# Performance work log

Measured on AMD Instinct MI355X. Metric: run time of the kernel, lower is better.

Reference implementation:

```python
import jax, jax.numpy as jnp
import numpy as np

B, C, L = 64, 128, 1024
SCALES = [8, 4, 2, 1]
EPS_BN = 1e-5


def _ema_vec(x_ds, alpha):
    # x_ds: [B, C, Ls]; alpha: [1, C, 1] in (0,1)
    Ls = x_ds.shape[-1]
    powers = jnp.arange(Ls - 1, -1, -1, dtype=x_ds.dtype)
    base = jnp.power(1.0 - alpha, powers)                                 # [1, C, Ls]
    w_num = jnp.concatenate([base[..., :1], base[..., 1:] * alpha], axis=-1)
    num = jnp.cumsum(x_ds * w_num, axis=-1)
    den = jnp.maximum(jnp.cumsum(base, axis=-1), 1e-12)
    return num / den


def _dwconv(x, w, s):
    # depthwise Conv1d: kernel 2s, stride s, pad s//2, groups=C, no bias
    return jax.lax.conv_general_dilated(
        x, w, window_strides=(s,), padding=[(s // 2, s // 2)],
        dimension_numbers=("NCH", "OIH", "NCH"), feature_group_count=C)


def _proj(v, w1, b1, w2, b2):
    # v: [B, C, Ls] -> Linear(Ls->L), exact GELU, Linear(L->L); torch Linear y = x @ W.T + b
    h = jax.nn.gelu(jnp.einsum("bcs,ls->bcl", v, w1) + b1, approximate=False)
    return jnp.einsum("bcl,ml->bcm", h, w2) + b2


def _hasd(x, bn_g, bn_b, branch, gate):
    Bn = x.shape[0]
    # BatchNorm1d over flattened (C*L) features, training-mode batch stats (biased var)
    v = x.reshape(Bn, C * L)
    mu = v.mean(axis=0)
    var = jnp.mean((v - mu) ** 2, axis=0)
    xn = (((v - mu) / jnp.sqrt(var + EPS_BN)) * bn_g + bn_b).reshape(Bn, C, L)
    trends, seasons, gates = [], [], []
    for s in SCALES:
        if s > 1:
            cw, w1, b1, w2, b2 = branch[s]
            down = _dwconv(xn, cw, s)                                     # [B, C, L//s]
            up = _proj(down, w1, b1, w2, b2)                              # [B, C, L]
        else:
            down = xn
            up = xn
        gw, gb, al = gate[s]
        alpha = jax.nn.sigmoid(al)
        trend_ds = _ema_vec(down, alpha)
        trend_up = _proj(trend_ds, w1, b1, w2, b2) if s > 1 else trend_ds
        season = up - trend_up
        trends.append(trend_up)
        seasons.append(season)
        gates.append(jax.nn.sigmoid(season.mean(axis=-1) @ gw.T + gb))    # [B, 1]
    g = jnp.concatenate(gates, axis=1)                                    # [B, n_scales]
    g = g / (g.sum(axis=1, keepdims=True) + 1e-6)
    g = g[:, :, None, None]
    trend_out = (jnp.stack(trends, axis=1) * g).sum(axis=1)
    season_out = (jnp.stack(seasons, axis=1) * g).sum(axis=1)
    return season_out, trend_out


def setup_inputs() -> dict:
    key = jax.random.key(0)
    ks = iter(jax.random.split(key, 64))
    d = {"x": jax.random.normal(next(ks), (B, C, L), jnp.float32)}
    d["bn_g"] = 1.0 + 0.1 * jax.random.normal(next(ks), (C * L,), jnp.float32)
    d["bn_b"] = 0.1 * jax.random.normal(next(ks), (C * L,), jnp.float32)
    for s in (8, 4, 2):
        Ls = L // s
        d[f"cw{s}"] = jax.random.normal(next(ks), (C, 1, 2 * s), jnp.float32) / np.sqrt(2 * s)
        d[f"w1_{s}"] = jax.random.normal(next(ks), (L, Ls), jnp.float32) / np.sqrt(Ls)
        d[f"b1_{s}"] = jnp.zeros((L,), jnp.float32)
        d[f"w2_{s}"] = jax.random.normal(next(ks), (L, L), jnp.float32) / np.sqrt(L)
        d[f"b2_{s}"] = jnp.zeros((L,), jnp.float32)
    for s in SCALES:
        d[f"gw{s}"] = jax.random.normal(next(ks), (1, C), jnp.float32) / np.sqrt(C)
        d[f"gb{s}"] = jnp.zeros((1,), jnp.float32)
        d[f"al{s}"] = jnp.full((1, C, 1), 0.3, jnp.float32)
    return d


def reference(x, bn_g, bn_b,
              cw8, w1_8, b1_8, w2_8, b2_8,
              cw4, w1_4, b1_4, w2_4, b2_4,
              cw2, w1_2, b1_2, w2_2, b2_2,
              gw8, gb8, al8, gw4, gb4, al4, gw2, gb2, al2, gw1, gb1, al1):
    branch = {8: (cw8, w1_8, b1_8, w2_8, b2_8),
              4: (cw4, w1_4, b1_4, w2_4, b2_4),
              2: (cw2, w1_2, b1_2, w2_2, b2_2)}
    gate = {8: (gw8, gb8, al8), 4: (gw4, gb4, al4),
            2: (gw2, gb2, al2), 1: (gw1, gb1, al1)}
    return _hasd(x, bn_g, bn_b, branch, gate)
```

## Files before the change

kernel.cpp:

```cpp
#include <hip/hip_runtime.h>
#include <hip/hip_bf16.h>
#include <math.h>

#define Bdim 64
#define Cdim 128
#define Ldim 1024
#define BC   (Bdim * Cdim)
#define CLn  (Cdim * Ldim)
#define TOT  (Bdim * CLn)

typedef unsigned short ushort_t;
typedef short s16x8 __attribute__((ext_vector_type(8)));
typedef float f32x4 __attribute__((ext_vector_type(4)));

__device__ __forceinline__ float bf2f(ushort_t u) {
    return __uint_as_float(((unsigned)u) << 16);
}
__device__ __forceinline__ ushort_t f2bf(float f) {
    __hip_bfloat16 h = __float2bfloat16(f);
    return *(ushort_t*)&h;
}
__device__ __forceinline__ void async16(const ushort_t* g, ushort_t* l) {
    __builtin_amdgcn_global_load_lds(
        (const __attribute__((address_space(1))) unsigned int*)g,
        (__attribute__((address_space(3))) unsigned int*)l, 16, 0, 0);
}
__device__ __forceinline__ float fast_gelu(float z) {
    float z2 = z * z;
    float inner = fmaf(0.044715f * z2, z, z);
    float e = __expf(-1.5957691216057308f * inner);
    return z * __builtin_amdgcn_rcpf(1.f + e);
}

#define PREP_CONV   15872
#define PREP_BN     (PREP_CONV + 512)
#define PREP_W2CS   (PREP_BN + 48)
#define PREP_COEF   (PREP_W2CS + 128)
#define PREP_TOTAL  (PREP_COEF + 128)

__global__ __launch_bounds__(256) void prep_kernel(
    const float* __restrict__ w1_8, const float* __restrict__ w1_4,
    const float* __restrict__ w1_2, const float* __restrict__ w2_8,
    const float* __restrict__ w2_4, const float* __restrict__ w2_2,
    ushort_t* __restrict__ wdst,
    const float* __restrict__ x, const float* __restrict__ bn_g,
    const float* __restrict__ bn_b, float* __restrict__ scale,
    float* __restrict__ shift,
    float* __restrict__ w2cs,
    const float* __restrict__ al1, const float* __restrict__ al2,
    const float* __restrict__ al4, const float* __restrict__ al8,
    float* __restrict__ coef, float* __restrict__ am,
    float* __restrict__ rs)
{
    __shared__ float red[4][64];
    int bid = blockIdx.x;
    int tid = threadIdx.x;

    if (bid < PREP_CONV) {
        int idx = bid * 256 + tid;
        const float* src; int off;
        if      (idx < 131072)  { src = w1_8; off = 0; }
        else if (idx < 393216)  { src = w1_4; off = 131072; }
        else if (idx < 917504)  { src = w1_2; off = 393216; }
        else if (idx < 1966080) { src = w2_8; off = 917504; }
        else if (idx < 3014656) { src = w2_4; off = 1966080; }
        else                    { src = w2_2; off = 3014656; }
        wdst[idx] = f2bf(src[idx - off]);
    } else if (bid < PREP_BN) {
        int f = (bid - PREP_CONV) * 256 + tid;
        float sum = 0.f, sumsq = 0.f;
        for (int b = 0; b < Bdim; ++b) {
            float v = x[(size_t)b * CLn + f];
            sum += v; sumsq += v * v;
        }
        float mu  = sum * (1.f / Bdim);
        float var = fmaxf(sumsq * (1.f / Bdim) - mu * mu, 0.f);
        float sc  = bn_g[f] / sqrtf(var + 1e-5f);
        scale[f] = sc;
        shift[f] = bn_b[f] - mu * sc;
    } else if (bid < PREP_W2CS) {
        int fl = bid - PREP_BN;
        int bx = fl & 15;
        int by = fl >> 4;
        const float* w = (by == 0) ? w2_8 : (by == 1) ? w2_4 : w2_2;
        int h  = bx * 64 + (tid & 63);
        int ls = tid >> 6;
        float s = 0.f;
        for (int l = ls; l < 1024; l += 4) s += w[(size_t)l * 1024 + h];
        red[ls][tid & 63] = s;
        __syncthreads();
        if (ls == 0)
            w2cs[by * 1024 + h] =
                red[0][tid] + red[1][tid] + red[2][tid] + red[3][tid];
    } else if (bid < PREP_COEF) {
        int c = bid - PREP_W2CS;
        const float* als[4] = {al1, al2, al4, al8};
        const int Lss[4]    = {1024, 512, 256, 128};
        const int offs[4]   = {0, 1024, 1536, 1792};
#pragma unroll
        for (int si = 0; si < 4; ++si) {
            double a  = 1.0 / (1.0 + exp(-(double)als[si][c]));
            double m  = 1.0 - a;
            double lm = log(m);
            int Ls = Lss[si];
            for (int t = tid; t < Ls; t += 256) {
                double dt  = (1.0 - exp((double)(t + 1) * lm)) / a;
                double den = exp((double)(Ls - 1 - t) * lm) * dt;
                double ramp = (den >= 1e-12) ? 1.0 : den * 1e12;
                coef[(size_t)c * 1920 + offs[si] + t] = (float)(ramp / dt);
            }
            if (tid == 0) {
                am[c * 8 + si * 2 + 0] = (float)a;
                am[c * 8 + si * 2 + 1] = (float)m;
            }
        }
    } else {
        int idx = (bid - PREP_COEF) * 256 + tid;
        rs[idx] = 0.f;
    }
}

template<int SEG>
__device__ __forceinline__ void ema_pass1(
    const float* __restrict__ src, float a, float m, bool lead,
    float* __restrict__ xs, float& Sp, float& Sm)
{
    int lane = threadIdx.x & 63;
    if constexpr (SEG >= 4) {
#pragma unroll
        for (int i = 0; i < SEG; i += 4) {
            f32x4 u = *(const f32x4*)&src[lane * SEG + i];
            xs[i + 0] = u.x; xs[i + 1] = u.y;
            xs[i + 2] = u.z; xs[i + 3] = u.w;
        }
    } else {
        float2 u = *(const float2*)&src[lane * 2];
        xs[0] = u.x; xs[1] = u.y;
    }
    float p = 0.f;
#pragma unroll
    for (int i = 0; i < SEG; ++i) {
        float bi = a * xs[i];
        if (lead && lane == 0 && i == 0) bi = xs[0];
        p = fmaf(m, p, bi);
    }
    float sm = m;
#pragma unroll
    for (int i = 1; i < SEG; ++i) sm *= m;
    Sp = p; Sm = sm;
#pragma unroll
    for (int d = 1; d < 64; d <<= 1) {
        float pm = __shfl_up(Sp, d);
        float mm = __shfl_up(Sm, d);
        if (lane >= d) { Sp = fmaf(Sm, pm, Sp); Sm *= mm; }
    }
}

template<int SEG, bool DIFF>
__device__ __forceinline__ float ema_pass2(
    const float* __restrict__ xs, float a, float m, bool lead, float carry,
    const float* __restrict__ cf, ushort_t* __restrict__ dst)
{
    int lane = threadIdx.x & 63;
    float y = carry, diff = 0.f;
    unsigned pk[(SEG + 1) / 2];
#pragma unroll
    for (int i = 0; i < SEG; ++i) {
        float bi = a * xs[i];
        if (lead && lane == 0 && i == 0) bi = xs[0];
        y = fmaf(m, y, bi);
        float tr = y * cf[lane * SEG + i];
        unsigned h = f2bf(tr);
        if ((i & 1) == 0) pk[i >> 1] = h;
        else              pk[i >> 1] |= h << 16;
        if (DIFF) diff += xs[i] - tr;
    }
    if constexpr (SEG == 8) {
        uint4 v; v.x = pk[0]; v.y = pk[1]; v.z = pk[2]; v.w = pk[3];
        *(uint4*)(dst + lane * 8) = v;
    } else if constexpr (SEG == 4) {
        uint2 v; v.x = pk[0]; v.y = pk[1];
        *(uint2*)(dst + lane * 4) = v;
    } else {
        *(unsigned*)(dst + lane * 2) = pk[0];
    }
    return diff;
}

__global__ __launch_bounds__(256) void pre_kernel(
    const float* __restrict__ x, const float* __restrict__ scale,
    const float* __restrict__ shift,
    const float* __restrict__ cw8, const float* __restrict__ cw4,
    const float* __restrict__ cw2,
    const float* __restrict__ coef, const float* __restrict__ amtab,
    ushort_t* __restrict__ xn_bf, ushort_t* __restrict__ t1_bf,
    ushort_t* __restrict__ A8, ushort_t* __restrict__ A4,
    ushort_t* __restrict__ A2, float* __restrict__ rs)
{
    __shared__ float sxn[1024];
    __shared__ float sxnp[1056];
    __shared__ float sconv[896];
    __shared__ float sP0;
    __shared__ float sdiff[2];
    int r   = blockIdx.x;
    int c   = r & (Cdim - 1);
    int tid = threadIdx.x;

    {
        const float* xr = x + (size_t)r * 1024;
        float4 xv = *(const float4*)(xr + tid * 4);
        float4 sc = *(const float4*)(scale + (size_t)c * 1024 + tid * 4);
        float4 sh = *(const float4*)(shift + (size_t)c * 1024 + tid * 4);
        float v0 = fmaf(xv.x, sc.x, sh.x);
        float v1 = fmaf(xv.y, sc.y, sh.y);
        float v2 = fmaf(xv.z, sc.z, sh.z);
        float v3 = fmaf(xv.w, sc.w, sh.w);
        int p = tid * 4;
        sxn[p + 0] = v0; sxn[p + 1] = v1; sxn[p + 2] = v2; sxn[p + 3] = v3;
        int pp = p + (p >> 5);
        sxnp[pp + 0] = v0; sxnp[pp + 1] = v1;
        sxnp[pp + 2] = v2; sxnp[pp + 3] = v3;
        uint2 pk;
        pk.x = (unsigned)f2bf(v0) | ((unsigned)f2bf(v1) << 16);
        pk.y = (unsigned)f2bf(v2) | ((unsigned)f2bf(v3) << 16);
        *(uint2*)(xn_bf + (size_t)r * 1024 + tid * 4) = pk;
    }
    __syncthreads();

    {
        const float* w2 = cw2 + c * 4;
        unsigned a2pk = 0;
#pragma unroll
        for (int j = 0; j < 2; ++j) {
            int o = tid * 2 + j;
            int start = o * 2 - 1;
            float acc = 0.f;
#pragma unroll
            for (int k = 0; k < 4; ++k) {
                int pos = start + k;
                float v = (pos >= 0 && pos < 1024) ? sxnp[pos + (pos >> 5)] : 0.f;
                acc = fmaf(v, w2[k], acc);
            }
            sconv[o] = acc;
            a2pk |= ((unsigned)f2bf(acc)) << (j * 16);
        }
        *(unsigned*)(A2 + (size_t)r * 512 + tid * 2) = a2pk;
        {
            const float* w4 = cw4 + c * 8;
            int o = tid;
            int start = o * 4 - 2;
            float acc = 0.f;
#pragma unroll
            for (int k = 0; k < 8; ++k) {
                int pos = start + k;
                float v = (pos >= 0 && pos < 1024) ? sxnp[pos + (pos >> 5)] : 0.f;
                acc = fmaf(v, w4[k], acc);
            }
            sconv[512 + o] = acc;
            A4[(size_t)r * 256 + o] = f2bf(acc);
        }
        if (tid < 128) {
            const float* w8 = cw8 + c * 16;
            int o = tid;
            int start = o * 8 - 4;
            float acc = 0.f;
#pragma unroll
            for (int k = 0; k < 16; ++k) {
                int pos = start + k;
                float v = (pos >= 0 && pos < 1024) ? sxnp[pos + (pos >> 5)] : 0.f;
                acc = fmaf(v, w8[k], acc);
            }
            sconv[768 + o] = acc;
            A8[(size_t)r * 128 + o] = f2bf(acc);
        }
    }
    __syncthreads();

    int wave = tid >> 6;
    int lane = tid & 63;
    const float* cf = coef + (size_t)c * 1920;
    const float* am = amtab + c * 8;
    float xs[8];
    float Sp = 0.f, Sm = 1.f, aE = 0.f, mE = 0.f;

    if (wave == 0) {
        aE = am[0]; mE = am[1];
        ema_pass1<8>(sxn, aE, mE, true, xs, Sp, Sm);
        if (lane == 63) sP0 = Sp;
    } else if (wave == 1) {
        aE = am[0]; mE = am[1];
        ema_pass1<8>(sxn + 512, aE, mE, false, xs, Sp, Sm);
    } else if (wave == 2) {
        aE = am[2]; mE = am[3];
        ema_pass1<8>(sconv, aE, mE, true, xs, Sp, Sm);
    } else {
        aE = am[4]; mE = am[5];
        ema_pass1<4>(sconv + 512, aE, mE, true, xs, Sp, Sm);
    }
    __syncthreads();

    float cs  = __shfl_up(Sp, 1);
    float msf = __shfl_up(Sm, 1);
    float carry = lane ? cs : 0.f;

    if (wave == 0) {
        float d = ema_pass2<8, true>(xs, aE, mE, true, carry,
                                     cf, t1_bf + (size_t)r * 1024);
#pragma unroll
        for (int dd = 32; dd; dd >>= 1) d += __shfl_down(d, dd);
        if (lane == 0) sdiff[0] = d;
    } else if (wave == 1) {
        carry += sP0 * (lane ? msf : 1.f);
        float d = ema_pass2<8, true>(xs, aE, mE, false, carry,
                                     cf + 512, t1_bf + (size_t)r * 1024 + 512);
#pragma unroll
        for (int dd = 32; dd; dd >>= 1) d += __shfl_down(d, dd);
        if (lane == 0) sdiff[1] = d;
    } else if (wave == 2) {
        ema_pass2<8, false>(xs, aE, mE, true, carry,
                            cf + 1024, A2 + ((size_t)BC + r) * 512);
    } else {
        ema_pass2<4, false>(xs, aE, mE, true, carry,
                            cf + 1536, A4 + ((size_t)BC + r) * 256);
        float xs2[2];
        aE = am[6]; mE = am[7];
        ema_pass1<2>(sconv + 768, aE, mE, true, xs2, Sp, Sm);
        float cs2 = __shfl_up(Sp, 1);
        float c2  = lane ? cs2 : 0.f;
        ema_pass2<2, false>(xs2, aE, mE, true, c2,
                            cf + 1792, A8 + ((size_t)BC + r) * 128);
    }
    __syncthreads();
    if (tid == 0) rs[3 * BC + r] = sdiff[0] + sdiff[1];
}

__global__ __launch_bounds__(256, 2) void gemm1_kernel(
    const ushort_t* __restrict__ Abase,
    const ushort_t* __restrict__ Wbase,
    const float* __restrict__ b1_8, const float* __restrict__ b1_4,
    const float* __restrict__ b1_2, const float* __restrict__ w2cs,
    ushort_t* __restrict__ Hbase, float* __restrict__ rs)
{
    int gx = blockIdx.x;
    int z  = 2 - (gx >> 6);
    int mi = gx & 63;
    int K = 128 << z;
    const ushort_t* A  = Abase + (size_t)2 * BC * 128 * ((1 << z) - 1);
    const ushort_t* Bw = Wbase + (size_t)131072 * ((1 << z) - 1);
    const float* bias  = (z == 0) ? b1_8 : (z == 1) ? b1_4 : b1_2;
    ushort_t* Hout     = Hbase + (size_t)z * 2 * TOT;

    __shared__ ushort_t Asu[128 * 64];
    __shared__ ushort_t Ast[128 * 64];
    __shared__ ushort_t Bs[128 * 64];
    int tid  = threadIdx.x;
    int wave = tid >> 6;
    int lane = tid & 63;
    int m0 = mi * 128, n0 = blockIdx.y * 128;
    int wm = (wave & 1) * 64, wn = (wave >> 1) * 64;
    int lrow = lane >> 3;
    int pc   = lane & 7;
    int fr   = lane & 15;
    int quad = lane >> 4;

    f32x4 accu[4][4], acct[4][4];
#pragma unroll
    for (int i = 0; i < 4; ++i)
#pragma unroll
        for (int j = 0; j < 4; ++j) {
            accu[i][j] = (f32x4){0.f, 0.f, 0.f, 0.f};
            acct[i][j] = (f32x4){0.f, 0.f, 0.f, 0.f};
        }

    for (int k0 = 0; k0 < K; k0 += 64) {
        __syncthreads();
#pragma unroll
        for (int i = 0; i < 4; ++i) {
            int rb  = wave * 32 + i * 8;
            int row = rb + lrow;
            int lc  = (pc - row) & 7;
            async16(A + (size_t)(m0 + row) * K + k0 + lc * 8,      &Asu[rb * 64]);
            async16(A + (size_t)(BC + m0 + row) * K + k0 + lc * 8, &Ast[rb * 64]);
            async16(Bw + (size_t)(n0 + row) * K + k0 + lc * 8,     &Bs[rb * 64]);
        }
        __syncthreads();
#pragma unroll
        for (int kk = 0; kk < 64; kk += 32) {
            s16x8 af[4], bfr[4];
            int lcA = (kk >> 3) + quad;
#pragma unroll
            for (int t = 0; t < 4; ++t) {
                int nr  = wn + t * 16 + fr;
                bfr[t] = *(const s16x8*)&Bs[nr * 64 + ((lcA + nr) & 7) * 8];
            }
#pragma unroll
            for (int t = 0; t < 4; ++t) {
                int mr  = wm + t * 16 + fr;
                af[t]  = *(const s16x8*)&Asu[mr * 64 + ((lcA + mr) & 7) * 8];
            }
#pragma unroll
            for (int mt = 0; mt < 4; ++mt)
#pragma unroll
                for (int nt = 0; nt < 4; ++nt)
                    accu[mt][nt] = __builtin_amdgcn_mfma_f32_16x16x32_bf16(
                        af[mt], bfr[nt], accu[mt][nt], 0, 0, 0);
#pragma unroll
            for (int t = 0; t < 4; ++t) {
                int mr  = wm + t * 16 + fr;
                af[t]  = *(const s16x8*)&Ast[mr * 64 + ((lcA + mr) & 7) * 8];
            }
#pragma unroll
            for (int mt = 0; mt < 4; ++mt)
#pragma unroll
                for (int nt = 0; nt < 4; ++nt)
                    acct[mt][nt] = __builtin_amdgcn_mfma_f32_16x16x32_bf16(
                        af[mt], bfr[nt], acct[mt][nt], 0, 0, 0);
        }
    }
    float racc[16];
#pragma unroll
    for (int e = 0; e < 16; ++e) racc[e] = 0.f;
#pragma unroll
    for (int mt = 0; mt < 4; ++mt)
#pragma unroll
        for (int nt = 0; nt < 4; ++nt) {
            int col = n0 + wn + nt * 16 + fr;
            float bcol = bias[col];
            float wcs = w2cs[z * 1024 + col];
#pragma unroll
            for (int rr = 0; rr < 4; ++rr) {
                size_t row = m0 + wm + mt * 16 + quad * 4 + rr;
                float gu = fast_gelu(accu[mt][nt][rr] + bcol);
                float gt = fast_gelu(acct[mt][nt][rr] + bcol);
                Hout[row * 1024 + col]        = f2bf(gu);
                Hout[(BC + row) * 1024 + col] = f2bf(gt);
                racc[mt * 4 + rr] = fmaf(gu - gt, wcs, racc[mt * 4 + rr]);
            }
        }
#pragma unroll
    for (int e = 0; e < 16; ++e) {
        float v = racc[e];
        v += __shfl_xor(v, 1); v += __shfl_xor(v, 2);
        v += __shfl_xor(v, 4); v += __shfl_xor(v, 8);
        if (fr == 0) {
            int mt = e >> 2, rr = e & 3;
            int row = m0 + wm + mt * 16 + quad * 4 + rr;
            atomicAdd(&rs[z * BC + row], v);
        }
    }
}

__global__ __launch_bounds__(256, 2) void gemm2_kernel(
    const ushort_t* __restrict__ Hbase,
    const ushort_t* __restrict__ W2base,
    const float* __restrict__ b2_8, const float* __restrict__ b2_4,
    const float* __restrict__ b2_2, const float* __restrict__ g,
    const ushort_t* __restrict__ t1_bf, const ushort_t* __restrict__ xn_bf,
    float* __restrict__ trend_out, float* __restrict__ season_out)
{
    __shared__ ushort_t Asu[128 * 64];
    __shared__ ushort_t Ast[128 * 64];
    __shared__ ushort_t Bs[128 * 64];
    int tid  = threadIdx.x;
    int wave = tid >> 6;
    int lane = tid & 63;
    int m0 = blockIdx.x * 128, n0 = blockIdx.y * 128;
    int wm = (wave & 1) * 64, wn = (wave >> 1) * 64;
    int lrow = lane >> 3;
    int pc   = lane & 7;
    int fr   = lane & 15;
    int quad = lane >> 4;
    int b = m0 >> 7;
    float gv0 = g[b * 4 + 0], gv1 = g[b * 4 + 1], gv2 = g[b * 4 + 2];
    float g1  = g[b * 4 + 3];
    float gsv[3] = {gv0, gv1, gv2};

    f32x4 accu[4][4], acct[4][4];
#pragma unroll
    for (int i = 0; i < 4; ++i)
#pragma unroll
        for (int j = 0; j < 4; ++j) {
            accu[i][j] = (f32x4){0.f, 0.f, 0.f, 0.f};
            acct[i][j] = (f32x4){0.f, 0.f, 0.f, 0.f};
        }

    for (int s = 0; s < 3; ++s) {
        if (s > 0) {
            float rr_ = gsv[s - 1] / fmaxf(gsv[s], 1e-30f);
#pragma unroll
            for (int mt = 0; mt < 4; ++mt)
#pragma unroll
                for (int nt = 0; nt < 4; ++nt)
#pragma unroll
                    for (int rr = 0; rr < 4; ++rr) {
                        accu[mt][nt][rr] *= rr_;
                        acct[mt][nt][rr] *= rr_;
                    }
        }
        const ushort_t* Au = Hbase + (size_t)s * 2 * TOT;
        const ushort_t* At = Au + TOT;
        const ushort_t* Bw = W2base + (size_t)s * 1048576;
        for (int k0 = 0; k0 < 1024; k0 += 64) {
            __syncthreads();
#pragma unroll
            for (int i = 0; i < 4; ++i) {
                int rb  = wave * 32 + i * 8;
                int row = rb + lrow;
                int lc  = (pc - row) & 7;
                size_t goff = (size_t)(m0 + row) * 1024 + k0 + lc * 8;
                async16(Au + goff, &Asu[rb * 64]);
                async16(At + goff, &Ast[rb * 64]);
                async16(Bw + (size_t)(n0 + row) * 1024 + k0 + lc * 8, &Bs[rb * 64]);
            }
            __syncthreads();
#pragma unroll
            for (int kk = 0; kk < 64; kk += 32) {
                s16x8 af[4], bfr[4];
                int lcA = (kk >> 3) + quad;
#pragma unroll
                for (int t = 0; t < 4; ++t) {
                    int nr  = wn + t * 16 + fr;
                    bfr[t] = *(const s16x8*)&Bs[nr * 64 + ((lcA + nr) & 7) * 8];
                }
#pragma unroll
                for (int t = 0; t < 4; ++t) {
                    int mr  = wm + t * 16 + fr;
                    af[t]  = *(const s16x8*)&Asu[mr * 64 + ((lcA + mr) & 7) * 8];
                }
#pragma unroll
                for (int mt = 0; mt < 4; ++mt)
#pragma unroll
                    for (int nt = 0; nt < 4; ++nt)
                        accu[mt][nt] = __builtin_amdgcn_mfma_f32_16x16x32_bf16(
                            af[mt], bfr[nt], accu[mt][nt], 0, 0, 0);
#pragma unroll
                for (int t = 0; t < 4; ++t) {
                    int mr  = wm + t * 16 + fr;
                    af[t]  = *(const s16x8*)&Ast[mr * 64 + ((lcA + mr) & 7) * 8];
                }
#pragma unroll
                for (int mt = 0; mt < 4; ++mt)
#pragma unroll
                    for (int nt = 0; nt < 4; ++nt)
                        acct[mt][nt] = __builtin_amdgcn_mfma_f32_16x16x32_bf16(
                            af[mt], bfr[nt], acct[mt][nt], 0, 0, 0);
            }
        }
    }
#pragma unroll
    for (int mt = 0; mt < 4; ++mt)
#pragma unroll
        for (int nt = 0; nt < 4; ++nt)
#pragma unroll
            for (int rr = 0; rr < 4; ++rr) {
                accu[mt][nt][rr] *= gv2;
                acct[mt][nt][rr] *= gv2;
            }

#pragma unroll
    for (int mt = 0; mt < 4; ++mt)
#pragma unroll
        for (int nt = 0; nt < 4; ++nt) {
            int col = n0 + wn + nt * 16 + fr;
            float cb2 = gv0 * b2_8[col] + gv1 * b2_4[col] + gv2 * b2_2[col];
#pragma unroll
            for (int r = 0; r < 4; ++r) {
                size_t row = m0 + wm + mt * 16 + quad * 4 + r;
                size_t idx = row * 1024 + col;
                float tr = acct[mt][nt][r] + cb2 + g1 * bf2f(t1_bf[idx]);
                float se = accu[mt][nt][r] + cb2 + g1 * bf2f(xn_bf[idx]) - tr;
                trend_out[idx]  = tr;
                season_out[idx] = se;
            }
        }
}

__global__ __launch_bounds__(128) void gate_kernel(
    const float* __restrict__ rs,
    const float* __restrict__ gw8, const float* __restrict__ gb8,
    const float* __restrict__ gw4, const float* __restrict__ gb4,
    const float* __restrict__ gw2, const float* __restrict__ gb2,
    const float* __restrict__ gw1, const float* __restrict__ gb1,
    float* __restrict__ g)
{
    int b = blockIdx.x;
    int c = threadIdx.x;
    const float* gws[4] = {gw8, gw4, gw2, gw1};
    const float* gbs[4] = {gb8, gb4, gb2, gb1};
    __shared__ float buf[128];
    __shared__ float gates[4];
    for (int si = 0; si < 4; ++si) {
        buf[c] = rs[si * BC + b * Cdim + c] * (1.f / Ldim) * gws[si][c];
        __syncthreads();
        for (int off = 64; off >= 1; off >>= 1) {
            if (c < off) buf[c] += buf[c + off];
            __syncthreads();
        }
        if (c == 0) {
            float z = buf[0] + gbs[si][0];
            gates[si] = 1.f / (1.f + expf(-z));
        }
        __syncthreads();
    }
    if (c == 0) {
        float s = gates[0] + gates[1] + gates[2] + gates[3] + 1e-6f;
#pragma unroll
        for (int si = 0; si < 4; ++si) g[b * 4 + si] = gates[si] / s;
    }
}

extern "C" void kernel_launch(void* const* d_in, const int* in_sizes, int n_in,
                              void* d_out, int out_size, void* d_ws, size_t ws_size,
                              hipStream_t stream)
{
    const float* x    = (const float*)d_in[0];
    const float* bn_g = (const float*)d_in[1];
    const float* bn_b = (const float*)d_in[2];
    const float* cw8  = (const float*)d_in[3];
    const float* w1_8 = (const float*)d_in[4];
    const float* b1_8 = (const float*)d_in[5];
    const float* w2_8 = (const float*)d_in[6];
    const float* b2_8 = (const float*)d_in[7];
    const float* cw4  = (const float*)d_in[8];
    const float* w1_4 = (const float*)d_in[9];
    const float* b1_4 = (const float*)d_in[10];
    const float* w2_4 = (const float*)d_in[11];
    const float* b2_4 = (const float*)d_in[12];
    const float* cw2  = (const float*)d_in[13];
    const float* w1_2 = (const float*)d_in[14];
    const float* b1_2 = (const float*)d_in[15];
    const float* w2_2 = (const float*)d_in[16];
    const float* b2_2 = (const float*)d_in[17];
    const float* gw8  = (const float*)d_in[18];
    const float* gb8  = (const float*)d_in[19];
    const float* al8  = (const float*)d_in[20];
    const float* gw4  = (const float*)d_in[21];
    const float* gb4  = (const float*)d_in[22];
    const float* al4  = (const float*)d_in[23];
    const float* gw2  = (const float*)d_in[24];
    const float* gb2  = (const float*)d_in[25];
    const float* al2  = (const float*)d_in[26];
    const float* gw1  = (const float*)d_in[27];
    const float* gb1  = (const float*)d_in[28];
    const float* al1  = (const float*)d_in[29];

    ushort_t* p_xn  = (ushort_t*)d_ws;
    ushort_t* p_t1  = p_xn + TOT;
    ushort_t* p_H   = p_t1 + TOT;
    ushort_t* p_wb  = p_H + 6 * (size_t)TOT;
    ushort_t* p_w1b = p_wb;
    ushort_t* p_w2b = p_wb + 917504;
    float*    p_sc  = (float*)(p_wb + 4063232);
    float*    p_sh  = p_sc + CLn;
    float*    p_w2cs = p_sh + CLn;
    float*    p_rs  = p_w2cs + 3 * 1024;
    float*    p_g   = p_rs + 4 * BC;
    float*    p_coef = (float*)p_H;
    float*    p_am   = p_coef + 128 * 1920;
    ushort_t* p_A8 = (ushort_t*)d_out;
    ushort_t* p_A4 = p_A8 + 2 * (size_t)BC * 128;
    ushort_t* p_A2 = p_A4 + 2 * (size_t)BC * 256;
    float*    p_season = (float*)d_out;
    float*    p_trend  = (float*)d_out + TOT;

    prep_kernel<<<PREP_TOTAL, 256, 0, stream>>>(
        w1_8, w1_4, w1_2, w2_8, w2_4, w2_2, p_wb,
        x, bn_g, bn_b, p_sc, p_sh,
        p_w2cs,
        al1, al2, al4, al8, p_coef, p_am,
        p_rs);

    pre_kernel<<<BC, 256, 0, stream>>>(x, p_sc, p_sh, cw8, cw4, cw2,
                                       p_coef, p_am,
                                       p_xn, p_t1, p_A8, p_A4, p_A2, p_rs);

    gemm1_kernel<<<dim3(192, 8), 256, 0, stream>>>(
        p_A8, p_w1b, b1_8, b1_4, b1_2, p_w2cs, p_H, p_rs);

    gate_kernel<<<Bdim, 128, 0, stream>>>(p_rs, gw8, gb8, gw4, gb4,
                                          gw2, gb2, gw1, gb1, p_g);

    gemm2_kernel<<<dim3(64, 8), 256, 0, stream>>>(
        p_H, p_w2b, b2_8, b2_4, b2_2, p_g, p_t1, p_xn, p_trend, p_season);
}
```

Measured before the change: 413.0 us.

## Restructure gemm2 into 512-thread double-buffered pipelined GEMM with wave-split u/t outputs

Rewrites the second GEMM kernel to use 512 threads with a 128x256 output tile. The u and t halves are stacked as 256 virtual A rows, with separate wave groups computing them, and results are exchanged through LDS in the epilogue. The global-to-LDS loads are double-buffered and issued in half-k stages, with explicit vmcnt waits, barriers, sched_barriers and setprio around the MFMA blocks, so memory traffic overlaps compute instead of the load-sync-compute pattern. The aim is to hide load latency and halve B reloads per block. The cost is 128KB of shared memory per block, fragile hand-tuned wait counts, and an extra LDS exchange for the season output.

Measured after the change: 420.8 us. No clear change (+1.9%).

```diff
diff --git a/kernel.cpp b/kernel.cpp
--- a/kernel.cpp
+++ b/kernel.cpp
@@ -450,7 +450,7 @@
     }
 }
 
-__global__ __launch_bounds__(256, 2) void gemm2_kernel(
+__global__ __launch_bounds__(512, 2) void gemm2_kernel(
     const ushort_t* __restrict__ Hbase,
     const ushort_t* __restrict__ W2base,
     const float* __restrict__ b2_8, const float* __restrict__ b2_4,
@@ -458,121 +458,198 @@
     const ushort_t* __restrict__ t1_bf, const ushort_t* __restrict__ xn_bf,
     float* __restrict__ trend_out, float* __restrict__ season_out)
 {
-    __shared__ ushort_t Asu[128 * 64];
-    __shared__ ushort_t Ast[128 * 64];
-    __shared__ ushort_t Bs[128 * 64];
+    __shared__ ushort_t smem[65536];
     int tid  = threadIdx.x;
     int wave = tid >> 6;
     int lane = tid & 63;
-    int m0 = blockIdx.x * 128, n0 = blockIdx.y * 128;
-    int wm = (wave & 1) * 64, wn = (wave >> 1) * 64;
-    int lrow = lane >> 3;
-    int pc   = lane & 7;
+    int m0 = blockIdx.x * 128;
+    int n0 = blockIdx.y * 256;
+    int wm   = wave >> 2;
+    int wn   = wave & 3;
+    int wm128 = wm * 128;
+    int rlow = lane >> 2;
+    int s4   = lane & 3;
     int fr   = lane & 15;
     int quad = lane >> 4;
-    int b = m0 >> 7;
-    float gv0 = g[b * 4 + 0], gv1 = g[b * 4 + 1], gv2 = g[b * 4 + 2];
-    float g1  = g[b * 4 + 3];
+    int bidx = blockIdx.x;
+    float gv0 = g[bidx * 4 + 0], gv1 = g[bidx * 4 + 1];
+    float gv2 = g[bidx * 4 + 2], g1 = g[bidx * 4 + 3];
     float gsv[3] = {gv0, gv1, gv2};
 
-    f32x4 accu[4][4], acct[4][4];
-#pragma unroll
-    for (int i = 0; i < 4; ++i)
-#pragma unroll
-        for (int j = 0; j < 4; ++j) {
-            accu[i][j] = (f32x4){0.f, 0.f, 0.f, 0.f};
-            acct[i][j] = (f32x4){0.f, 0.f, 0.f, 0.f};
-        }
-
-    for (int s = 0; s < 3; ++s) {
-        if (s > 0) {
+    f32x4 acc[8][4];
+#pragma unroll
+    for (int i = 0; i < 8; ++i)
+#pragma unroll
+        for (int j = 0; j < 4; ++j) acc[i][j] = (f32x4){0.f, 0.f, 0.f, 0.f};
+
+    auto stageA = [&](int t, int ksub) {
+        if (t >= 48) return;
+        int s = t >> 4;
+        int k0e = (t & 15) * 64 + ksub * 32;
+        ushort_t* dstb = smem + (t & 1) * 32768 + ksub * 8192;
+#pragma unroll
+        for (int i = 0; i < 2; ++i) {
+            int vr = wave * 32 + i * 16 + rlow;
+            int cg = (s4 - (vr >> 1)) & 3;
+            const ushort_t* src = Hbase + (size_t)s * 2 * TOT
+                + (size_t)(vr >> 7) * TOT
+                + (size_t)(m0 + (vr & 127)) * 1024 + k0e + cg * 8;
+            async16(src, dstb + (wave * 32 + i * 16) * 32);
+        }
+    };
+    auto stageB = [&](int t, int ksub) {
+        if (t >= 48) return;
+        int s = t >> 4;
+        int k0e = (t & 15) * 64 + ksub * 32;
+        ushort_t* dstb = smem + (t & 1) * 32768 + 16384 + ksub * 8192;
+#pragma unroll
+        for (int i = 0; i < 2; ++i) {
+            int vr = wave * 32 + i * 16 + rlow;
+            int cg = (s4 - (vr >> 1)) & 3;
+            const ushort_t* src = W2base + (size_t)s * 1048576
+                + (size_t)(n0 + vr) * 1024 + k0e + cg * 8;
+            async16(src, dstb + (wave * 32 + i * 16) * 32);
+        }
+    };
+
+    stageA(0, 0); stageB(0, 0);
+    stageA(0, 1); stageB(0, 1);
+    stageA(1, 0); stageB(1, 0);
+
+    s16x8 af[4], bf[4];
+    for (int kt = 0; kt < 48; ++kt) {
+        if (kt == 16 || kt == 32) {
+            int s = kt >> 4;
             float rr_ = gsv[s - 1] / fmaxf(gsv[s], 1e-30f);
 #pragma unroll
-            for (int mt = 0; mt < 4; ++mt)
-#pragma unroll
-                for (int nt = 0; nt < 4; ++nt)
-#pragma unroll
-                    for (int rr = 0; rr < 4; ++rr) {
-                        accu[mt][nt][rr] *= rr_;
-                        acct[mt][nt][rr] *= rr_;
-                    }
-        }
-        const ushort_t* Au = Hbase + (size_t)s * 2 * TOT;
-        const ushort_t* At = Au + TOT;
-        const ushort_t* Bw = W2base + (size_t)s * 1048576;
-        for (int k0 = 0; k0 < 1024; k0 += 64) {
-            __syncthreads();
-#pragma unroll
-            for (int i = 0; i < 4; ++i) {
-                int rb  = wave * 32 + i * 8;
-                int row = rb + lrow;
-                int lc  = (pc - row) & 7;
-                size_t goff = (size_t)(m0 + row) * 1024 + k0 + lc * 8;
-                async16(Au + goff, &Asu[rb * 64]);
-                async16(At + goff, &Ast[rb * 64]);
-                async16(Bw + (size_t)(n0 + row) * 1024 + k0 + lc * 8, &Bs[rb * 64]);
-            }
-            __syncthreads();
-#pragma unroll
-            for (int kk = 0; kk < 64; kk += 32) {
-                s16x8 af[4], bfr[4];
-                int lcA = (kk >> 3) + quad;
-#pragma unroll
-                for (int t = 0; t < 4; ++t) {
-                    int nr  = wn + t * 16 + fr;
-                    bfr[t] = *(const s16x8*)&Bs[nr * 64 + ((lcA + nr) & 7) * 8];
+            for (int i = 0; i < 8; ++i)
+#pragma unroll
+                for (int j = 0; j < 4; ++j)
+#pragma unroll
+                    for (int e = 0; e < 4; ++e) acc[i][j][e] *= rr_;
+        }
+        const ushort_t* Ab = smem + (kt & 1) * 32768;
+        const ushort_t* Bb = Ab + 16384;
+
+        if (kt < 47) { asm volatile("s_waitcnt vmcnt(8)" ::: "memory"); }
+        else         { asm volatile("s_waitcnt vmcnt(4)" ::: "memory"); }
+        __builtin_amdgcn_s_barrier();
+        __builtin_amdgcn_sched_barrier(0);
+#pragma unroll
+        for (int q = 0; q < 4; ++q) {
+            int vrA = wm128 + q * 16 + fr;
+            af[q] = *(const s16x8*)&Ab[vrA * 32 + ((quad + (vrA >> 1)) & 3) * 8];
+            int vrB = wn * 64 + q * 16 + fr;
+            bf[q] = *(const s16x8*)&Bb[vrB * 32 + ((quad + (vrB >> 1)) & 3) * 8];
+        }
+        stageA(kt + 1, 1);
+        __builtin_amdgcn_s_setprio(1);
+#pragma unroll
+        for (int mt = 0; mt < 4; ++mt)
+#pragma unroll
+            for (int nt = 0; nt < 4; ++nt)
+                acc[mt][nt] = __builtin_amdgcn_mfma_f32_16x16x32_bf16(
+                    af[mt], bf[nt], acc[mt][nt], 0, 0, 0);
+        __builtin_amdgcn_s_setprio(0);
+        __builtin_amdgcn_sched_barrier(0);
+
+        __builtin_amdgcn_s_barrier();
+        __builtin_amdgcn_sched_barrier(0);
+#pragma unroll
+        for (int q = 0; q < 4; ++q) {
+            int vrA = wm128 + (4 + q) * 16 + fr;
+            af[q] = *(const s16x8*)&Ab[vrA * 32 + ((quad + (vrA >> 1)) & 3) * 8];
+        }
+        stageB(kt + 1, 1);
+        __builtin_amdgcn_s_setprio(1);
+#pragma unroll
+        for (int mt = 0; mt < 4; ++mt)
+#pragma unroll
+            for (int nt = 0; nt < 4; ++nt)
+                acc[4 + mt][nt] = __builtin_amdgcn_mfma_f32_16x16x32_bf16(
+                    af[mt], bf[nt], acc[4 + mt][nt], 0, 0, 0);
+        __builtin_amdgcn_s_setprio(0);
+        __builtin_amdgcn_sched_barrier(0);
+
+        if (kt < 47) { asm volatile("s_waitcnt vmcnt(8)" ::: "memory"); }
+        else         { asm volatile("s_waitcnt vmcnt(0)" ::: "memory"); }
+        __builtin_amdgcn_s_barrier();
+        __builtin_amdgcn_sched_barrier(0);
+#pragma unroll
+        for (int q = 0; q < 4; ++q) {
+            int vrA = wm128 + q * 16 + fr;
+            af[q] = *(const s16x8*)&Ab[8192 + vrA * 32 + ((quad + (vrA >> 1)) & 3) * 8];
+            int vrB = wn * 64 + q * 16 + fr;
+            bf[q] = *(const s16x8*)&Bb[8192 + vrB * 32 + ((quad + (vrB >> 1)) & 3) * 8];
+        }
+        stageA(kt + 2, 0);
+        __builtin_amdgcn_s_setprio(1);
+#pragma unroll
+        for (int mt = 0; mt < 4; ++mt)
+#pragma unroll
+            for (int nt = 0; nt < 4; ++nt)
+                acc[mt][nt] = __builtin_amdgcn_mfma_f32_16x16x32_bf16(
+                    af[mt], bf[nt], acc[mt][nt], 0, 0, 0);
+        __builtin_amdgcn_s_setprio(0);
+        __builtin_amdgcn_sched_barrier(0);
+
+        __builtin_amdgcn_s_barrier();
+        __builtin_amdgcn_sched_barrier(0);
+#pragma unroll
+        for (int q = 0; q < 4; ++q) {
+            int vrA = wm128 + (4 + q) * 16 + fr;
+            af[q] = *(const s16x8*)&Ab[8192 + vrA * 32 + ((quad + (vrA >> 1)) & 3) * 8];
+        }
+        stageB(kt + 2, 0);
+        __builtin_amdgcn_s_setprio(1);
+#pragma unroll
+        for (int mt = 0; mt < 4; ++mt)
+#pragma unroll
+            for (int nt = 0; nt < 4; ++nt)
+                acc[4 + mt][nt] = __builtin_amdgcn_mfma_f32_16x16x32_bf16(
+                    af[mt], bf[nt], acc[4 + mt][nt], 0, 0, 0);
+        __builtin_amdgcn_s_setprio(0);
+        __builtin_amdgcn_sched_barrier(0);
+    }
+
+    __syncthreads();
+    float* exch = (float*)smem;
+    if (wm == 1) {
+#pragma unroll
+        for (int f = 0; f < 8; ++f)
+#pragma unroll
+            for (int j = 0; j < 4; ++j) {
+                int col = n0 + wn * 64 + j * 16 + fr;
+                float cb2 = gv0 * b2_8[col] + gv1 * b2_4[col] + gv2 * b2_2[col];
+#pragma unroll
+                for (int rr = 0; rr < 4; ++rr) {
+                    int lrow = f * 16 + quad * 4 + rr;
+                    size_t idx = (size_t)(m0 + lrow) * 1024 + col;
+                    float tr = acc[f][j][rr] * gv2 + cb2 + g1 * bf2f(t1_bf[idx]);
+                    trend_out[idx] = tr;
+                    exch[wn * 8192 + lrow * 64 + j * 16 + fr] = tr;
                 }
-#pragma unroll
-                for (int t = 0; t < 4; ++t) {
-                    int mr  = wm + t * 16 + fr;
-                    af[t]  = *(const s16x8*)&Asu[mr * 64 + ((lcA + mr) & 7) * 8];
+            }
+    }
+    __syncthreads();
+    if (wm == 0) {
+#pragma unroll
+        for (int f = 0; f < 8; ++f)
+#pragma unroll
+            for (int j = 0; j < 4; ++j) {
+                int col = n0 + wn * 64 + j * 16 + fr;
+                float cb2 = gv0 * b2_8[col] + gv1 * b2_4[col] + gv2 * b2_2[col];
+#pragma unroll
+                for (int rr = 0; rr < 4; ++rr) {
+                    int lrow = f * 16 + quad * 4 + rr;
+                    size_t idx = (size_t)(m0 + lrow) * 1024 + col;
+                    float tr = exch[wn * 8192 + lrow * 64 + j * 16 + fr];
+                    float se = acc[f][j][rr] * gv2 + cb2
+                             + g1 * bf2f(xn_bf[idx]) - tr;
+                    season_out[idx] = se;
                 }
-#pragma unroll
-                for (int mt = 0; mt < 4; ++mt)
-#pragma unroll
-                    for (int nt = 0; nt < 4; ++nt)
-                        accu[mt][nt] = __builtin_amdgcn_mfma_f32_16x16x32_bf16(
-                            af[mt], bfr[nt], accu[mt][nt], 0, 0, 0);
-#pragma unroll
-                for (int t = 0; t < 4; ++t) {
-                    int mr  = wm + t * 16 + fr;
-                    af[t]  = *(const s16x8*)&Ast[mr * 64 + ((lcA + mr) & 7) * 8];
-                }
-#pragma unroll
-                for (int mt = 0; mt < 4; ++mt)
-#pragma unroll
-                    for (int nt = 0; nt < 4; ++nt)
-                        acct[mt][nt] = __builtin_amdgcn_mfma_f32_16x16x32_bf16(
-                            af[mt], bfr[nt], acct[mt][nt], 0, 0, 0);
-            }
-        }
-    }
-#pragma unroll
-    for (int mt = 0; mt < 4; ++mt)
-#pragma unroll
-        for (int nt = 0; nt < 4; ++nt)
-#pragma unroll
-            for (int rr = 0; rr < 4; ++rr) {
-                accu[mt][nt][rr] *= gv2;
-                acct[mt][nt][rr] *= gv2;
-            }
-
-#pragma unroll
-    for (int mt = 0; mt < 4; ++mt)
-#pragma unroll
-        for (int nt = 0; nt < 4; ++nt) {
-            int col = n0 + wn + nt * 16 + fr;
-            float cb2 = gv0 * b2_8[col] + gv1 * b2_4[col] + gv2 * b2_2[col];
-#pragma unroll
-            for (int r = 0; r < 4; ++r) {
-                size_t row = m0 + wm + mt * 16 + quad * 4 + r;
-                size_t idx = row * 1024 + col;
-                float tr = acct[mt][nt][r] + cb2 + g1 * bf2f(t1_bf[idx]);
-                float se = accu[mt][nt][r] + cb2 + g1 * bf2f(xn_bf[idx]) - tr;
-                trend_out[idx]  = tr;
-                season_out[idx] = se;
-            }
-        }
+            }
+    }
 }
 
 __global__ __launch_bounds__(128) void gate_kernel(
@@ -680,6 +757,6 @@
     gate_kernel<<<Bdim, 128, 0, stream>>>(p_rs, gw8, gb8, gw4, gb4,
                                           gw2, gb2, gw1, gb1, p_g);
 
-    gemm2_kernel<<<dim3(64, 8), 256, 0, stream>>>(
+    gemm2_kernel<<<dim3(64, 4), 512, 0, stream>>>(
         p_H, p_w2b, b2_8, b2_4, b2_2, p_g, p_t1, p_xn, p_trend, p_season);
 }
```
